# Kernel optimization log

Measured on AMD Instinct MI355X. Metric: run time of the kernel, lower is better.

The kernel has to match this reference:

```python
import jax, jax.numpy as jnp
import numpy as np

N_NODES = 50000
N_EDGES = 800000
D_IN = 64   # input_dimension + 1
D_HID = 64


def _gcn_conv(x, src, dst, W, b, deg_isqrt):
    # PyG GCNConv: X' = D^{-1/2} (A + I) D^{-1/2} X W + b
    h = x @ W  # [N, H]
    norm = (deg_isqrt[src] * deg_isqrt[dst])[:, None]  # [E, 1]
    agg = jax.ops.segment_sum(h[src] * norm, dst, num_segments=x.shape[0])
    # self-loop contribution: norm_ii = deg_isqrt[i]^2
    agg = agg + h * (deg_isqrt * deg_isqrt)[:, None]
    return agg + b


def setup_inputs() -> dict:
    key = jax.random.key(0)
    ks = jax.random.split(key, 8)
    x = jax.random.normal(ks[0], (N_NODES, D_IN), dtype=jnp.float32)
    edge_index = jax.random.randint(ks[1], (2, N_EDGES), 0, N_NODES, dtype=jnp.int32)
    s = 1.0 / np.sqrt(D_HID)
    W0 = jax.random.normal(ks[2], (D_IN, D_HID), dtype=jnp.float32) * s
    b0 = jnp.zeros((D_HID,), dtype=jnp.float32)
    W1 = jax.random.normal(ks[3], (D_HID, D_HID), dtype=jnp.float32) * s
    b1 = jnp.zeros((D_HID,), dtype=jnp.float32)
    W2 = jax.random.normal(ks[4], (D_HID, D_HID), dtype=jnp.float32) * s
    b2 = jnp.zeros((D_HID,), dtype=jnp.float32)
    Wout = jax.random.normal(ks[5], (D_HID, 1), dtype=jnp.float32) * s
    bout = jnp.zeros((1,), dtype=jnp.float32)
    return {"x": x, "edge_index": edge_index, "W0": W0, "b0": b0,
            "W1": W1, "b1": b1, "W2": W2, "b2": b2,
            "Wout": Wout, "bout": bout}


def reference(x, edge_index, W0, b0, W1, b1, W2, b2, Wout, bout):
    src, dst = edge_index[0], edge_index[1]
    n = x.shape[0]
    # degree with self-loop (edge weight 1.0 each)
    deg = jnp.zeros((n,), x.dtype).at[dst].add(1.0) + 1.0
    deg_isqrt = jax.lax.rsqrt(deg)
    h = jax.nn.relu(_gcn_conv(x, src, dst, W0, b0, deg_isqrt))
    h = jax.nn.relu(_gcn_conv(h, src, dst, W1, b1, deg_isqrt))
    h = jax.nn.relu(_gcn_conv(h, src, dst, W2, b2, deg_isqrt))
    return h @ Wout + bout  # [N, 1]
```

## Files before the change

### kernel.cpp

```cpp
#include <hip/hip_runtime.h>
#include <hip/hip_bf16.h>

#define D 64
#define N_NODES 50000
#define N_EDGES 800000
#define TILE 16

__global__ void hist_k(const int* __restrict__ dst, int* __restrict__ cnt, int E) {
    int i = blockIdx.x * blockDim.x + threadIdx.x;
    if (i < E) atomicAdd(&cnt[dst[i]], 1);
}

__global__ void scan1_k(const int* __restrict__ cnt, int* __restrict__ off,
                        int* __restrict__ bsum, float* __restrict__ dis, int N) {
    __shared__ int sh[256];
    int t = threadIdx.x;
    int i = blockIdx.x * 256 + t;
    int v = (i < N) ? cnt[i] : 0;
    sh[t] = v;
    __syncthreads();
#pragma unroll
    for (int d = 1; d < 256; d <<= 1) {
        int u = (t >= d) ? sh[t - d] : 0;
        __syncthreads();
        sh[t] += u;
        __syncthreads();
    }
    if (i < N) {
        off[i] = sh[t] - v;
        dis[i] = rsqrtf((float)v + 1.0f);
    }
    if (t == 255) bsum[blockIdx.x] = sh[255];
}

__global__ void scan2_k(int* __restrict__ bsum, int nb) {
    __shared__ int sh[256];
    int t = threadIdx.x;
    int v = (t < nb) ? bsum[t] : 0;
    sh[t] = v;
    __syncthreads();
#pragma unroll
    for (int d = 1; d < 256; d <<= 1) {
        int u = (t >= d) ? sh[t - d] : 0;
        __syncthreads();
        sh[t] += u;
        __syncthreads();
    }
    if (t < nb) bsum[t] = sh[t] - v;
}

__global__ void scan3_k(int* __restrict__ off, const int* __restrict__ bsum,
                        int* __restrict__ cursor, int N, int E) {
    int i = blockIdx.x * 256 + threadIdx.x;
    if (i < N) {
        int o = off[i] + bsum[blockIdx.x];
        off[i] = o;
        cursor[i] = o;
    }
    if (i == 0) off[N] = E;
}

__device__ __forceinline__ void fma4(float4& a, float s, float4 w) {
    a.x = fmaf(s, w.x, a.x);
    a.y = fmaf(s, w.y, a.y);
    a.z = fmaf(s, w.z, a.z);
    a.w = fmaf(s, w.w, a.w);
}

__device__ __forceinline__ void tile_gemm(const float (*hbuf)[68], const float4* __restrict__ W4,
                                          const float* __restrict__ dis, float* __restrict__ outp,
                                          int base, int t) {
    int lane = t & 63;
    int cg = lane & 15;
    int rr = (t >> 6) * 4 + (lane >> 4);
    float4 acc = make_float4(0.f, 0.f, 0.f, 0.f);
#pragma unroll
    for (int kk = 0; kk < 16; ++kk) {
        float4 hb = *(const float4*)&hbuf[rr][kk * 4];
        fma4(acc, hb.x, W4[(kk * 4 + 0) * 16 + cg]);
        fma4(acc, hb.y, W4[(kk * 4 + 1) * 16 + cg]);
        fma4(acc, hb.z, W4[(kk * 4 + 2) * 16 + cg]);
        fma4(acc, hb.w, W4[(kk * 4 + 3) * 16 + cg]);
    }
    float dv = dis[base + rr];
    acc.x *= dv; acc.y *= dv; acc.z *= dv; acc.w *= dv;
    ((float4*)outp)[(size_t)(base + rr) * 16 + cg] = acc;
}

__global__ void fused0_k(const float4* __restrict__ X4, const float4* __restrict__ W4,
                         const float* __restrict__ dis, float* __restrict__ H,
                         const int* __restrict__ src, const int* __restrict__ dst,
                         int* __restrict__ cursor, int* __restrict__ esrc,
                         int N, int E, int gemmBlocks) {
    __shared__ float hbuf[TILE][68];
    int bid = blockIdx.x;
    int t = threadIdx.x;
    if (bid < gemmBlocks) {
        int base = bid * TILE;
        int r = t >> 4, ch = t & 15;
        float4 v = X4[(size_t)(base + r) * 16 + ch];
        *(float4*)&hbuf[r][ch * 4] = v;
        __syncthreads();
        tile_gemm(hbuf, W4, dis, H, base, t);
    } else {
        int fb = bid - gemmBlocks;
        int nfb = gridDim.x - gemmBlocks;
        for (int i = fb * 256 + threadIdx.x; i < E; i += nfb * 256) {
            int pos = atomicAdd(&cursor[dst[i]], 1);
            esrc[pos] = src[i];
        }
    }
}

template <int FINAL>
__global__ void layer_k(const float4* __restrict__ Hs4, const int* __restrict__ off,
                        const int* __restrict__ esrc, const float* __restrict__ dis,
                        const float* __restrict__ bias, const float4* __restrict__ W4,
                        const float* __restrict__ bout, float* __restrict__ outp, int N) {
    __shared__ float hbuf[TILE][68];
    int t = threadIdx.x;
    int lane = t & 63;
    int w = t >> 6;
    int g = lane >> 4;
    int l16 = lane & 15;
    int rloc = w * 4 + g;
    int n = blockIdx.x * TILE + rloc;

    int beg = off[n], end = off[n + 1];
    float4 acc = Hs4[(size_t)n * 16 + l16];
    int j = beg;
    for (; j + 3 < end; j += 4) {
        int s0 = esrc[j], s1 = esrc[j + 1], s2 = esrc[j + 2], s3 = esrc[j + 3];
        float4 v0 = Hs4[(size_t)s0 * 16 + l16];
        float4 v1 = Hs4[(size_t)s1 * 16 + l16];
        float4 v2 = Hs4[(size_t)s2 * 16 + l16];
        float4 v3 = Hs4[(size_t)s3 * 16 + l16];
        acc.x += (v0.x + v1.x) + (v2.x + v3.x);
        acc.y += (v0.y + v1.y) + (v2.y + v3.y);
        acc.z += (v0.z + v1.z) + (v2.z + v3.z);
        acc.w += (v0.w + v1.w) + (v2.w + v3.w);
    }
    for (; j < end; ++j) {
        float4 v = Hs4[(size_t)esrc[j] * 16 + l16];
        acc.x += v.x; acc.y += v.y; acc.z += v.z; acc.w += v.w;
    }

    float dv = dis[n];
    float4 b4 = ((const float4*)bias)[l16];
    float4 h4;
    h4.x = fmaxf(fmaf(acc.x, dv, b4.x), 0.f);
    h4.y = fmaxf(fmaf(acc.y, dv, b4.y), 0.f);
    h4.z = fmaxf(fmaf(acc.z, dv, b4.z), 0.f);
    h4.w = fmaxf(fmaf(acc.w, dv, b4.w), 0.f);

    if (FINAL) {
        float4 w4 = ((const float4*)W4)[l16];
        float p = fmaf(h4.x, w4.x, fmaf(h4.y, w4.y, fmaf(h4.z, w4.z, h4.w * w4.w)));
        p += __shfl_xor(p, 1, 64);
        p += __shfl_xor(p, 2, 64);
        p += __shfl_xor(p, 4, 64);
        p += __shfl_xor(p, 8, 64);
        if (l16 == 0) outp[n] = p + bout[0];
    } else {
        *(float4*)&hbuf[rloc][l16 * 4] = h4;
        __syncthreads();
        tile_gemm(hbuf, W4, dis, outp, blockIdx.x * TILE, t);
    }
}

extern "C" void kernel_launch(void* const* d_in, const int* in_sizes, int n_in,
                              void* d_out, int out_size, void* d_ws, size_t ws_size,
                              hipStream_t stream) {
    const float* x    = (const float*)d_in[0];
    const int*   ei   = (const int*)d_in[1];
    const float* W0   = (const float*)d_in[2];
    const float* b0   = (const float*)d_in[3];
    const float* W1   = (const float*)d_in[4];
    const float* b1   = (const float*)d_in[5];
    const float* W2   = (const float*)d_in[6];
    const float* b2   = (const float*)d_in[7];
    const float* Wout = (const float*)d_in[8];
    const float* bout = (const float*)d_in[9];
    float* out = (float*)d_out;

    const int N = N_NODES, E = N_EDGES;
    const int* src = ei;
    const int* dst = ei + E;

    char* ws = (char*)d_ws;
    int*   cnt    = (int*)(ws);
    int*   off    = (int*)(ws + (256u << 10));
    int*   cursor = (int*)(ws + (512u << 10));
    float* dis    = (float*)(ws + (768u << 10));
    int*   bsum   = (int*)(ws + (990u << 10));
    int*   esrc   = (int*)(ws + (1u << 20));
    float* bufA   = (float*)(ws + (5u << 20));
    float* bufB   = (float*)(ws + (18u << 20));

    dim3 blk(256);
    const int NB = (N + 255) / 256;
    dim3 gN(NB);
    dim3 gE((E + 255) / 256);
    const int TILES = N / TILE;
    dim3 gTile(TILES);
    const int FILL_BLOCKS = 1024;

    hipMemsetAsync(cnt, 0, (size_t)N * sizeof(int), stream);
    hist_k<<<gE, blk, 0, stream>>>(dst, cnt, E);
    scan1_k<<<gN, blk, 0, stream>>>(cnt, off, bsum, dis, N);
    scan2_k<<<1, blk, 0, stream>>>(bsum, NB);
    scan3_k<<<gN, blk, 0, stream>>>(off, bsum, cursor, N, E);

    fused0_k<<<dim3(TILES + FILL_BLOCKS), blk, 0, stream>>>(
        (const float4*)x, (const float4*)W0, dis, bufA, src, dst, cursor, esrc,
        N, E, TILES);

    layer_k<0><<<gTile, blk, 0, stream>>>((const float4*)bufA, off, esrc, dis,
                                          b0, (const float4*)W1, nullptr, bufB, N);
    layer_k<0><<<gTile, blk, 0, stream>>>((const float4*)bufB, off, esrc, dis,
                                          b1, (const float4*)W2, nullptr, bufA, N);
    layer_k<1><<<gTile, blk, 0, stream>>>((const float4*)bufA, off, esrc, dis,
                                          b2, (const float4*)Wout, bout, out, N);
}
```

Measured before the change: 322.6 us.

## Overlap first GEMM with histogram, move degree scaling into fill kernel

The layer-0 X·W0 GEMM now runs alongside the degree histogram in one kernel, since the GEMM no longer needs dis. The degree scaling is applied later in a separate pass fused with the CSR fill kernel. The fill kernel also gets more blocks, and the gather loop is unrolled from 4 to 8 neighbours for more memory-level parallelism. The cost is an extra read-modify-write pass over H and higher register pressure in the layer kernel.

```diff
diff --git a/kernel.cpp b/kernel.cpp
--- a/kernel.cpp
+++ b/kernel.cpp
@@ -5,11 +5,6 @@
 #define N_NODES 50000
 #define N_EDGES 800000
 #define TILE 16
-
-__global__ void hist_k(const int* __restrict__ dst, int* __restrict__ cnt, int E) {
-    int i = blockIdx.x * blockDim.x + threadIdx.x;
-    if (i < E) atomicAdd(&cnt[dst[i]], 1);
-}
 
 __global__ void scan1_k(const int* __restrict__ cnt, int* __restrict__ off,
                         int* __restrict__ bsum, float* __restrict__ dis, int N) {
@@ -67,6 +62,7 @@
     a.w = fmaf(s, w.w, a.w);
 }
 
+template <int SCALED>
 __device__ __forceinline__ void tile_gemm(const float (*hbuf)[68], const float4* __restrict__ W4,
                                           const float* __restrict__ dis, float* __restrict__ outp,
                                           int base, int t) {
@@ -82,16 +78,16 @@
         fma4(acc, hb.z, W4[(kk * 4 + 2) * 16 + cg]);
         fma4(acc, hb.w, W4[(kk * 4 + 3) * 16 + cg]);
     }
-    float dv = dis[base + rr];
-    acc.x *= dv; acc.y *= dv; acc.z *= dv; acc.w *= dv;
+    if (SCALED) {
+        float dv = dis[base + rr];
+        acc.x *= dv; acc.y *= dv; acc.z *= dv; acc.w *= dv;
+    }
     ((float4*)outp)[(size_t)(base + rr) * 16 + cg] = acc;
 }
 
-__global__ void fused0_k(const float4* __restrict__ X4, const float4* __restrict__ W4,
-                         const float* __restrict__ dis, float* __restrict__ H,
-                         const int* __restrict__ src, const int* __restrict__ dst,
-                         int* __restrict__ cursor, int* __restrict__ esrc,
-                         int N, int E, int gemmBlocks) {
+__global__ void fused_pre_k(const float4* __restrict__ X4, const float4* __restrict__ W4,
+                            float* __restrict__ H, const int* __restrict__ dst,
+                            int* __restrict__ cnt, int N, int E, int gemmBlocks) {
     __shared__ float hbuf[TILE][68];
     int bid = blockIdx.x;
     int t = threadIdx.x;
@@ -101,13 +97,36 @@
         float4 v = X4[(size_t)(base + r) * 16 + ch];
         *(float4*)&hbuf[r][ch * 4] = v;
         __syncthreads();
-        tile_gemm(hbuf, W4, dis, H, base, t);
+        tile_gemm<0>(hbuf, W4, nullptr, H, base, t);
     } else {
-        int fb = bid - gemmBlocks;
-        int nfb = gridDim.x - gemmBlocks;
-        for (int i = fb * 256 + threadIdx.x; i < E; i += nfb * 256) {
+        int hb = bid - gemmBlocks;
+        int nhb = gridDim.x - gemmBlocks;
+        for (int i = hb * 256 + t; i < E; i += nhb * 256) {
+            atomicAdd(&cnt[dst[i]], 1);
+        }
+    }
+}
+
+__global__ void fused_fill_k(const int* __restrict__ src, const int* __restrict__ dst,
+                             int* __restrict__ cursor, int* __restrict__ esrc,
+                             float4* __restrict__ H4, const float* __restrict__ dis,
+                             int N, int E, int fillBlocks) {
+    int bid = blockIdx.x;
+    int t = threadIdx.x;
+    if (bid < fillBlocks) {
+        for (int i = bid * 256 + t; i < E; i += fillBlocks * 256) {
             int pos = atomicAdd(&cursor[dst[i]], 1);
             esrc[pos] = src[i];
+        }
+    } else {
+        int sb = bid - fillBlocks;
+        int nsb = gridDim.x - fillBlocks;
+        int total = N * 16;
+        for (int i = sb * 256 + t; i < total; i += nsb * 256) {
+            float4 v = H4[i];
+            float dv = dis[i >> 4];
+            v.x *= dv; v.y *= dv; v.z *= dv; v.w *= dv;
+            H4[i] = v;
         }
     }
 }
@@ -129,16 +148,21 @@
     int beg = off[n], end = off[n + 1];
     float4 acc = Hs4[(size_t)n * 16 + l16];
     int j = beg;
-    for (; j + 3 < end; j += 4) {
-        int s0 = esrc[j], s1 = esrc[j + 1], s2 = esrc[j + 2], s3 = esrc[j + 3];
+    for (; j + 7 < end; j += 8) {
+        int s0 = esrc[j],     s1 = esrc[j + 1], s2 = esrc[j + 2], s3 = esrc[j + 3];
+        int s4 = esrc[j + 4], s5 = esrc[j + 5], s6 = esrc[j + 6], s7 = esrc[j + 7];
         float4 v0 = Hs4[(size_t)s0 * 16 + l16];
         float4 v1 = Hs4[(size_t)s1 * 16 + l16];
         float4 v2 = Hs4[(size_t)s2 * 16 + l16];
         float4 v3 = Hs4[(size_t)s3 * 16 + l16];
-        acc.x += (v0.x + v1.x) + (v2.x + v3.x);
-        acc.y += (v0.y + v1.y) + (v2.y + v3.y);
-        acc.z += (v0.z + v1.z) + (v2.z + v3.z);
-        acc.w += (v0.w + v1.w) + (v2.w + v3.w);
+        float4 v4 = Hs4[(size_t)s4 * 16 + l16];
+        float4 v5 = Hs4[(size_t)s5 * 16 + l16];
+        float4 v6 = Hs4[(size_t)s6 * 16 + l16];
+        float4 v7 = Hs4[(size_t)s7 * 16 + l16];
+        acc.x += ((v0.x + v1.x) + (v2.x + v3.x)) + ((v4.x + v5.x) + (v6.x + v7.x));
+        acc.y += ((v0.y + v1.y) + (v2.y + v3.y)) + ((v4.y + v5.y) + (v6.y + v7.y));
+        acc.z += ((v0.z + v1.z) + (v2.z + v3.z)) + ((v4.z + v5.z) + (v6.z + v7.z));
+        acc.w += ((v0.w + v1.w) + (v2.w + v3.w)) + ((v4.w + v5.w) + (v6.w + v7.w));
     }
     for (; j < end; ++j) {
         float4 v = Hs4[(size_t)esrc[j] * 16 + l16];
@@ -164,7 +188,7 @@
     } else {
         *(float4*)&hbuf[rloc][l16 * 4] = h4;
         __syncthreads();
-        tile_gemm(hbuf, W4, dis, outp, blockIdx.x * TILE, t);
+        tile_gemm<1>(hbuf, W4, dis, outp, blockIdx.x * TILE, t);
     }
 }
 
@@ -200,20 +224,22 @@
     dim3 blk(256);
     const int NB = (N + 255) / 256;
     dim3 gN(NB);
-    dim3 gE((E + 255) / 256);
     const int TILES = N / TILE;
     dim3 gTile(TILES);
-    const int FILL_BLOCKS = 1024;
+    const int HIST_BLOCKS = 1563;
+    const int FILL_BLOCKS = 3125;
+    const int SCALE_BLOCKS = 784;
 
     hipMemsetAsync(cnt, 0, (size_t)N * sizeof(int), stream);
-    hist_k<<<gE, blk, 0, stream>>>(dst, cnt, E);
+    fused_pre_k<<<dim3(TILES + HIST_BLOCKS), blk, 0, stream>>>(
+        (const float4*)x, (const float4*)W0, bufA, dst, cnt, N, E, TILES);
+
     scan1_k<<<gN, blk, 0, stream>>>(cnt, off, bsum, dis, N);
     scan2_k<<<1, blk, 0, stream>>>(bsum, NB);
     scan3_k<<<gN, blk, 0, stream>>>(off, bsum, cursor, N, E);
 
-    fused0_k<<<dim3(TILES + FILL_BLOCKS), blk, 0, stream>>>(
-        (const float4*)x, (const float4*)W0, dis, bufA, src, dst, cursor, esrc,
-        N, E, TILES);
+    fused_fill_k<<<dim3(FILL_BLOCKS + SCALE_BLOCKS), blk, 0, stream>>>(
+        src, dst, cursor, esrc, (float4*)bufA, dis, N, E, FILL_BLOCKS);
 
     layer_k<0><<<gTile, blk, 0, stream>>>((const float4*)bufA, off, esrc, dis,
                                           b0, (const float4*)W1, nullptr, bufB, N);
```

New measurement: 314.6 us. -2.5%, faster.
